# Performance work log

Hardware: AMD Instinct MI355X
Metric: run time of the kernel (lower is better)

The kernel has to match this reference:

```python
import jax, jax.numpy as jnp
import numpy as np

N_NODES = 50000
N_EDGES = 1600000
N_GRAPHS = 16
K_SLOTS = 8
LATENT = 4
HID = 32


def _linear(key, fan_in, fan_out):
    lim = 1.0 / np.sqrt(fan_in)
    kw, kb = jax.random.split(key)
    w = jax.random.uniform(kw, (fan_in, fan_out), minval=-lim, maxval=lim, dtype=jnp.float32)
    b = jax.random.uniform(kb, (fan_out,), minval=-lim, maxval=lim, dtype=jnp.float32)
    return w, b


def setup_inputs() -> dict:
    key = jax.random.key(0)
    ks = jax.random.split(key, 12)
    x = jax.random.normal(ks[0], (N_NODES, 4), dtype=jnp.float32)
    pos = jax.random.normal(ks[1], (N_NODES, 3), dtype=jnp.float32)
    # edge_index without self-loops (src != dst) so dist > 0 everywhere
    src = jax.random.randint(ks[2], (N_EDGES,), 0, N_NODES)
    off = jax.random.randint(ks[3], (N_EDGES,), 1, N_NODES)
    dst = (src + off) % N_NODES
    edge_index = jnp.stack([src, dst], axis=0).astype(jnp.int64)
    batch = jnp.sort(jax.random.randint(ks[4], (N_NODES,), 0, N_GRAPHS)).astype(jnp.int64)
    enc_w1, enc_b1 = _linear(ks[5], 4 * 2 + 1, HID)
    enc_w2, enc_b2 = _linear(ks[6], HID, HID)
    pool_w, pool_b = _linear(ks[7], HID, K_SLOTS)
    toz_w, toz_b = _linear(ks[8], HID, LATENT)
    dec_w1, dec_b1 = _linear(ks[9], LATENT, HID)
    dec_w2, dec_b2 = _linear(ks[10], HID, 4)
    return {
        "x": x, "pos": pos, "edge_index": edge_index, "batch": batch,
        "enc_w1": enc_w1, "enc_b1": enc_b1, "enc_w2": enc_w2, "enc_b2": enc_b2,
        "pool_w": pool_w, "pool_b": pool_b, "toz_w": toz_w, "toz_b": toz_b,
        "dec_w1": dec_w1, "dec_b1": dec_b1, "dec_w2": dec_w2, "dec_b2": dec_b2,
    }


def reference(x, pos, edge_index, batch,
              enc_w1, enc_b1, enc_w2, enc_b2,
              pool_w, pool_b, toz_w, toz_b,
              dec_w1, dec_b1, dec_w2, dec_b2):
    src = edge_index[0]  # x_j (source)
    dst = edge_index[1]  # x_i (target, aggregation index in PyG default flow)
    # EquiLayer: relative distance + message MLP + mean aggregation
    rel_pos = pos[src] - pos[dst]                         # [E, 3]
    dist = jnp.linalg.norm(rel_pos, axis=-1, keepdims=True)  # [E, 1]
    msg_in = jnp.concatenate([x[dst], x[src], dist], axis=-1)  # [E, 9]
    msg = jax.nn.silu(msg_in @ enc_w1 + enc_b1) @ enc_w2 + enc_b2  # [E, 32]
    summed = jax.ops.segment_sum(msg, dst, num_segments=N_NODES)   # [N, 32]
    cnt = jax.ops.segment_sum(jnp.ones((msg.shape[0], 1), msg.dtype), dst,
                              num_segments=N_NODES)
    h = summed / jnp.maximum(cnt, 1.0)                    # scatter-mean
    # soft pooling over k slots per graph
    s = jax.nn.softmax(h @ pool_w + pool_b, axis=-1)      # [N, k]
    pooled_h = jax.ops.segment_sum(s[:, :, None] * h[:, None, :], batch,
                                   num_segments=N_GRAPHS)  # [B, k, 32]
    z = pooled_h @ toz_w + toz_b                           # [B, k, latent]
    # decode: torch.matmul(s [N,k], z [B,k,d]) -> [B, N, d]
    q = jnp.einsum('nk,bkd->bnd', s, z)
    recon = jax.nn.silu(q @ dec_w1 + dec_b1) @ dec_w2 + dec_b2  # [B, N, 4]
    return recon
```

## Files before the change

### kernel.cpp

```cpp
#include <hip/hip_runtime.h>
#include <hip/hip_bf16.h>

#define N_NODES 50000
#define N_EDGES 1600000
#define N_GRAPHS 16
#define K_SLOTS 8
#define LATENT 4
#define HID 32
#define NBUCKET 196
#define BCAP 10240
#define BIN_EPB 4096

typedef __hip_bfloat16 bf16;
typedef __attribute__((ext_vector_type(8))) short short8;
typedef __attribute__((ext_vector_type(4))) float f32x4;

__device__ __forceinline__ float ldf(const void* p, long i, int isbf) {
    return isbf ? __bfloat162float(((const bf16*)p)[i]) : ((const float*)p)[i];
}
__device__ __forceinline__ int ldi(const int* p, long i, int is64) {
    return is64 ? p[2 * i] : p[i];
}
__device__ __forceinline__ short f2bs(float f) {
    bf16 h = __float2bfloat16(f);
    return *reinterpret_cast<short*>(&h);
}
__device__ __forceinline__ unsigned pk2(float a, float b) {
    __hip_bfloat162 h2 = __float22bfloat162_rn(make_float2(a, b));
    return *reinterpret_cast<unsigned*>(&h2);
}
__device__ __forceinline__ float bs2f(unsigned s) {
    union { unsigned u; float f; } cv;
    cv.u = (s & 0xFFFFu) << 16;
    return cv.f;
}
__device__ __forceinline__ float fast_silu(float v) {
    return v * __builtin_amdgcn_rcpf(1.f + __expf(-v));
}

#define WS_POOL 0
#define WS_GFILL 4096
#define WS_ZERO_CNT 4352
#define WS_HSUM 4352
#define WS_S    (WS_HSUM + N_NODES * HID)
#define WS_FRAGS (WS_S + N_NODES * K_SLOTS)
#define WS_DEG  (WS_FRAGS + 1024)
#define WS_BINNED (WS_DEG + N_NODES)
#define WS_EDAT (WS_BINNED + NBUCKET * BCAP)
#define WS_FLAGS (WS_EDAT + N_EDGES)

__global__ void prep_kernel(const void* x, const int* ei,
                            const void* w1, const void* w2,
                            int* flags, short* frags)
{
    int t = threadIdx.x;
    unsigned short h = ((const unsigned short*)x)[2 * t];
    unsigned e = (h >> 7) & 0xFF;
    bool sane = ((h & 0x7FFF) == 0 || (e >= 100 && e <= 141));
    unsigned long long bs = __ballot(sane);
    int f0 = (__popcll(bs) >= 32) ? 1 : 0;
    bool z = (ei[2 * t + 1] == 0);
    unsigned long long bz = __ballot(z);
    int f1 = (__popcll(bz) >= 60) ? 1 : 0;
    if (t == 0) { flags[0] = f0; flags[1] = f1; }

    int fbf = f0;
    int nl = t & 15, quad = (t >> 4) & 3;
#pragma unroll
    for (int j = 0; j < 8; j++) {
        int k = quad * 8 + j;
        frags[(0 * 64 + t) * 8 + j] = (k < 9) ? f2bs(ldf(w1, k * 32 + nl, fbf)) : (short)0;
        frags[(1 * 64 + t) * 8 + j] = (k < 9) ? f2bs(ldf(w1, k * 32 + 16 + nl, fbf)) : (short)0;
        frags[(2 * 64 + t) * 8 + j] = f2bs(ldf(w2, k * 32 + nl, fbf));
        frags[(3 * 64 + t) * 8 + j] = f2bs(ldf(w2, k * 32 + 16 + nl, fbf));
    }
}

__global__ __launch_bounds__(256) void bin_kernel(
    const int* __restrict__ ei, int* __restrict__ gfill,
    unsigned* __restrict__ binned, const int* __restrict__ flags)
{
    const int i64 = flags[1];
    __shared__ int cnt[NBUCKET];
    __shared__ int lbase[NBUCKET];
    __shared__ int lcur[NBUCKET];
    __shared__ int gbase[NBUCKET];
    __shared__ int tmp[256];
    __shared__ unsigned sorted[BIN_EPB];
    int t = threadIdx.x;
    for (int i = t; i < NBUCKET; i += 256) cnt[i] = 0;
    __syncthreads();

    long e0 = (long)blockIdx.x * BIN_EPB;
    unsigned pk[16];
    if (!i64) {
#pragma unroll
        for (int kk = 0; kk < 4; kk++) {
            long e = e0 + kk * 1024 + t * 4;
            if (e < N_EDGES) {
                int4 sv = *(const int4*)(ei + e);
                int4 dv = *(const int4*)(ei + N_EDGES + e);
                pk[kk * 4 + 0] = (unsigned)sv.x | ((unsigned)dv.x << 16);
                pk[kk * 4 + 1] = (unsigned)sv.y | ((unsigned)dv.y << 16);
                pk[kk * 4 + 2] = (unsigned)sv.z | ((unsigned)dv.z << 16);
                pk[kk * 4 + 3] = (unsigned)sv.w | ((unsigned)dv.w << 16);
                atomicAdd(&cnt[dv.x >> 8], 1);
                atomicAdd(&cnt[dv.y >> 8], 1);
                atomicAdd(&cnt[dv.z >> 8], 1);
                atomicAdd(&cnt[dv.w >> 8], 1);
            } else {
                pk[kk * 4 + 0] = pk[kk * 4 + 1] = pk[kk * 4 + 2] = pk[kk * 4 + 3] = 0xFFFFFFFFu;
            }
        }
    } else {
#pragma unroll
        for (int kk = 0; kk < 8; kk++) {
            long e = e0 + kk * 512 + t * 2;
            if (e < N_EDGES) {
                int4 sv = *(const int4*)(ei + 2 * e);
                int4 dv = *(const int4*)(ei + 2 * (N_EDGES + e));
                pk[kk * 2 + 0] = (unsigned)sv.x | ((unsigned)dv.x << 16);
                pk[kk * 2 + 1] = (unsigned)sv.z | ((unsigned)dv.z << 16);
                atomicAdd(&cnt[dv.x >> 8], 1);
                atomicAdd(&cnt[dv.z >> 8], 1);
            } else {
                pk[kk * 2 + 0] = pk[kk * 2 + 1] = 0xFFFFFFFFu;
            }
        }
    }
    __syncthreads();

    tmp[t] = (t < NBUCKET) ? cnt[t] : 0;
    __syncthreads();
    for (int s = 1; s < 256; s <<= 1) {
        int v = tmp[t] + ((t >= s) ? tmp[t - s] : 0);
        __syncthreads();
        tmp[t] = v;
        __syncthreads();
    }
    int total = tmp[255];
    if (t < NBUCKET) {
        int ex = tmp[t] - cnt[t];
        lbase[t] = ex;
        lcur[t] = ex;
        gbase[t] = atomicAdd(&gfill[t], cnt[t]);
    }
    __syncthreads();

#pragma unroll
    for (int k = 0; k < 16; k++) {
        if (pk[k] != 0xFFFFFFFFu) {
            int b = pk[k] >> 24;
            int p = atomicAdd(&lcur[b], 1);
            sorted[p] = pk[k];
        }
    }
    __syncthreads();

    for (int j = t; j < total; j += 256) {
        unsigned ed = sorted[j];
        int b = ed >> 24;
        binned[(long)b * BCAP + gbase[b] + (j - lbase[b])] = ed;
    }
}

__global__ __launch_bounds__(1024) void csr_kernel(
    const int* __restrict__ gfill, const unsigned* __restrict__ binned,
    unsigned* __restrict__ edat, int* __restrict__ deg, float* __restrict__ hsum)
{
    __shared__ int gsm[256];
    __shared__ int lcnt[256], lcur[256], sm[256];
    int b = blockIdx.x, t = threadIdx.x;
    if (t < 256) gsm[t] = (t < NBUCKET) ? gfill[t] : 0;
    if (t < 256) lcnt[t] = 0;
    __syncthreads();
    for (int s = 1; s < 256; s <<= 1) {
        int v = 0;
        if (t < 256) v = gsm[t] + ((t >= s) ? gsm[t - s] : 0);
        __syncthreads();
        if (t < 256) gsm[t] = v;
        __syncthreads();
    }
    {
        int nvalid = min(256, N_NODES - b * 256);
        if (nvalid > 0) {
            float4* hz = (float4*)(hsum + (size_t)b * 256 * HID);
            float4 z4 = make_float4(0.f, 0.f, 0.f, 0.f);
            for (int i = t; i < nvalid * 8; i += 1024) hz[i] = z4;
        }
    }
    int cnt = gfill[b];
    int base = gsm[b] - cnt;
    const unsigned* bp = binned + (long)b * BCAP;
    for (int i = t; i < cnt; i += 1024)
        atomicAdd(&lcnt[(bp[i] >> 16) & 255], 1);
    __syncthreads();
    if (t < 256) sm[t] = lcnt[t];
    __syncthreads();
    for (int s = 1; s < 256; s <<= 1) {
        int v = 0;
        if (t < 256) v = sm[t] + ((t >= s) ? sm[t - s] : 0);
        __syncthreads();
        if (t < 256) sm[t] = v;
        __syncthreads();
    }
    if (t < 256) {
        lcur[t] = sm[t] - lcnt[t];
        int n = b * 256 + t;
        if (n < N_NODES) deg[n] = lcnt[t];
    }
    __syncthreads();
    for (int i = t; i < cnt; i += 1024) {
        unsigned pk = bp[i];
        int pos = base + atomicAdd(&lcur[(pk >> 16) & 255], 1);
        edat[pos] = pk;
    }
}

__global__ __launch_bounds__(256) void msg_agg_kernel(
    const void* __restrict__ x, const void* __restrict__ pos,
    const unsigned* __restrict__ edat, const short* __restrict__ frags,
    const void* __restrict__ b1, const void* __restrict__ b2,
    float* __restrict__ hsum, const int* __restrict__ flags)
{
    const int fbf = flags[0];
    __shared__ short buf[256 * 34];
    __shared__ int sdL[256];
    __shared__ int runstart[256];
    __shared__ int wcnt[4];

    int t = threadIdx.x;
    int lane = t & 63, wv = t >> 6;
    int nl = lane & 15, quad = lane >> 4;

    const short8 w1f0 = *(const short8*)&frags[(0 * 64 + lane) * 8];
    const short8 w1f1 = *(const short8*)&frags[(1 * 64 + lane) * 8];
    const short8 w2f0 = *(const short8*)&frags[(2 * 64 + lane) * 8];
    const short8 w2f1 = *(const short8*)&frags[(3 * 64 + lane) * 8];
    float b1c0 = ldf(b1, nl, fbf), b1c1 = ldf(b1, 16 + nl, fbf);
    float b2c0 = ldf(b2, nl, fbf), b2c1 = ldf(b2, 16 + nl, fbf);

    long i = (long)blockIdx.x * 256 + t;
    unsigned ed = edat[i];
    int src = (int)(ed & 0xFFFFu);
    int dst = (int)(ed >> 16);
    sdL[t] = dst;

    float in[9];
    if (fbf) {
        const unsigned* xb = (const unsigned*)x;
        unsigned d0 = xb[dst * 2], d1 = xb[dst * 2 + 1];
        unsigned s0 = xb[src * 2], s1 = xb[src * 2 + 1];
        in[0] = bs2f(d0); in[1] = bs2f(d0 >> 16);
        in[2] = bs2f(d1); in[3] = bs2f(d1 >> 16);
        in[4] = bs2f(s0); in[5] = bs2f(s0 >> 16);
        in[6] = bs2f(s1); in[7] = bs2f(s1 >> 16);
        const unsigned short* pp = (const unsigned short*)pos;
        float dx = bs2f(pp[3 * src + 0]) - bs2f(pp[3 * dst + 0]);
        float dy = bs2f(pp[3 * src + 1]) - bs2f(pp[3 * dst + 1]);
        float dz = bs2f(pp[3 * src + 2]) - bs2f(pp[3 * dst + 2]);
        in[8] = sqrtf(dx * dx + dy * dy + dz * dz);
    } else {
        float4 xd = ((const float4*)x)[dst];
        float4 xs = ((const float4*)x)[src];
        in[0] = xd.x; in[1] = xd.y; in[2] = xd.z; in[3] = xd.w;
        in[4] = xs.x; in[5] = xs.y; in[6] = xs.z; in[7] = xs.w;
        const float* pf = (const float*)pos;
        float dx = pf[3 * src + 0] - pf[3 * dst + 0];
        float dy = pf[3 * src + 1] - pf[3 * dst + 1];
        float dz = pf[3 * src + 2] - pf[3 * dst + 2];
        in[8] = sqrtf(dx * dx + dy * dy + dz * dz);
    }

    {
        unsigned* rowp = (unsigned*)&buf[t * 34];
        rowp[0] = pk2(in[0], in[1]);
        rowp[1] = pk2(in[2], in[3]);
        rowp[2] = pk2(in[4], in[5]);
        rowp[3] = pk2(in[6], in[7]);
        rowp[4] = pk2(in[8], 0.f);
#pragma unroll
        for (int p = 5; p < 16; p++) rowp[p] = 0;
    }
    __syncthreads();

    int rb = wv * 64;
    short8 af[4];
#pragma unroll
    for (int mt = 0; mt < 4; mt++) {
        int row = rb + mt * 16 + nl;
        af[mt] = *(short8*)&buf[row * 34 + quad * 8];
    }
    __syncthreads();

    f32x4 zero = {0.f, 0.f, 0.f, 0.f};
#pragma unroll
    for (int mt = 0; mt < 4; mt++) {
        f32x4 c0 = __builtin_amdgcn_mfma_f32_16x16x32_bf16(af[mt], w1f0, zero, 0, 0, 0);
        f32x4 c1 = __builtin_amdgcn_mfma_f32_16x16x32_bf16(af[mt], w1f1, zero, 0, 0, 0);
#pragma unroll
        for (int r = 0; r < 4; r++) {
            int row = rb + mt * 16 + quad * 4 + r;
            buf[row * 34 + nl] = f2bs(fast_silu(c0[r] + b1c0));
            buf[row * 34 + 16 + nl] = f2bs(fast_silu(c1[r] + b1c1));
        }
    }
    __syncthreads();

    short8 a2f[4];
#pragma unroll
    for (int mt = 0; mt < 4; mt++) {
        int row = rb + mt * 16 + nl;
        a2f[mt] = *(short8*)&buf[row * 34 + quad * 8];
    }
    __syncthreads();

    short* msgT = buf;
#pragma unroll
    for (int mt = 0; mt < 4; mt++) {
        f32x4 d0 = __builtin_amdgcn_mfma_f32_16x16x32_bf16(a2f[mt], w2f0, zero, 0, 0, 0);
        f32x4 d1 = __builtin_amdgcn_mfma_f32_16x16x32_bf16(a2f[mt], w2f1, zero, 0, 0, 0);
        int ob = rb + mt * 16 + quad * 4;
        unsigned* c0p = (unsigned*)&msgT[nl * 258 + ob];
        unsigned* c1p = (unsigned*)&msgT[(nl + 16) * 258 + ob];
        c0p[0] = pk2(d0[0] + b2c0, d0[1] + b2c0);
        c0p[1] = pk2(d0[2] + b2c0, d0[3] + b2c0);
        c1p[0] = pk2(d1[0] + b2c1, d1[1] + b2c1);
        c1p[1] = pk2(d1[2] + b2c1, d1[3] + b2c1);
    }
    __syncthreads();

    bool head = (t == 0) || (sdL[t] != sdL[t - 1]);
    unsigned long long bal = __ballot(head);
    if (lane == 0) wcnt[wv] = __popcll(bal);
    __syncthreads();
    int nruns = wcnt[0] + wcnt[1] + wcnt[2] + wcnt[3];
    if (head) {
        int base = 0;
        for (int q = 0; q < wv; q++) base += wcnt[q];
        int myrun = base + __popcll(bal & (((unsigned long long)1 << lane) - 1ull));
        runstart[myrun] = t;
    }
    __syncthreads();

    int g = t >> 5, c = t & 31;
    const short* col = &msgT[c * 258];
    const unsigned* colu = (const unsigned*)col;
    for (int r = g; r < nruns; r += 8) {
        int s0 = runstart[r];
        int s1 = (r + 1 < nruns) ? runstart[r + 1] : 256;
        float acc = 0.f;
        int j = s0;
        if (j & 1) { acc += bs2f((unsigned)(unsigned short)col[j]); j++; }
        for (; j + 1 < s1; j += 2) {
            unsigned d = colu[j >> 1];
            acc += bs2f(d) + bs2f(d >> 16);
        }
        if (j < s1) acc += bs2f((unsigned)(unsigned short)col[j]);
        int node = sdL[s0];
        if (s0 == 0 || s1 == 256) atomicAdd(&hsum[(size_t)node * HID + c], acc);
        else hsum[(size_t)node * HID + c] = acc;
    }
}

__global__ __launch_bounds__(256) void pool_softmax_kernel(
    const float* __restrict__ hsum, const int* __restrict__ deg,
    const int* __restrict__ batch,
    const void* __restrict__ pw, const void* __restrict__ pb,
    float* __restrict__ s, float* __restrict__ pooled,
    const int* __restrict__ flags)
{
    const int fbf = flags[0], i64 = flags[1];
    __shared__ float spw[HID * K_SLOTS], spb[K_SLOTS];
    __shared__ float hL[256 * 33];
    __shared__ float sL[256 * 9];
    __shared__ float invL[256];
    __shared__ int gL[256];
    int t = threadIdx.x;
    int n0 = blockIdx.x * 256;
    spw[t] = ldf(pw, t, fbf);
    if (t < K_SLOTS) spb[t] = ldf(pb, t, fbf);
    {
        int n = n0 + t;
        gL[t] = ldi(batch, (n < N_NODES) ? n : (N_NODES - 1), i64);
        invL[t] = (n < N_NODES) ? __builtin_amdgcn_rcpf(fmaxf((float)deg[n], 1.f)) : 0.f;
    }
    __syncthreads();
    for (int i = t; i < 256 * HID; i += 256) {
        int row = i >> 5, col = i & 31;
        int n = n0 + row;
        hL[row * 33 + col] = (n < N_NODES) ? hsum[(size_t)n0 * HID + i] * invL[row] : 0.f;
    }
    __syncthreads();

    if (n0 + t < N_NODES) {
        float l[K_SLOTS];
#pragma unroll
        for (int k = 0; k < K_SLOTS; k++) l[k] = spb[k];
#pragma unroll
        for (int j = 0; j < HID; j++) {
            float v = hL[t * 33 + j];
#pragma unroll
            for (int k = 0; k < K_SLOTS; k++) l[k] = fmaf(v, spw[j * K_SLOTS + k], l[k]);
        }
        float mx = l[0];
#pragma unroll
        for (int k = 1; k < K_SLOTS; k++) mx = fmaxf(mx, l[k]);
        float sum = 0.f;
#pragma unroll
        for (int k = 0; k < K_SLOTS; k++) { l[k] = __expf(l[k] - mx); sum += l[k]; }
        float is = __builtin_amdgcn_rcpf(sum);
#pragma unroll
        for (int k = 0; k < K_SLOTS; k++) { l[k] *= is; sL[t * 9 + k] = l[k]; }
        float4 v0 = make_float4(l[0], l[1], l[2], l[3]);
        float4 v1 = make_float4(l[4], l[5], l[6], l[7]);
        float4* sp = (float4*)(s + (size_t)(n0 + t) * K_SLOTS);
        sp[0] = v0; sp[1] = v1;
    } else {
#pragma unroll
        for (int k = 0; k < K_SLOTS; k++) sL[t * 9 + k] = 0.f;
    }
    __syncthreads();

    int k = t >> 5, c = t & 31;
    float acc = 0.f;
    int curg = gL[0];
    int lim = min(256, N_NODES - n0);
    for (int i = 0; i < lim; i++) {
        int g = gL[i];
        if (g != curg) {
            atomicAdd(&pooled[curg * 256 + t], acc);
            acc = 0.f;
            curg = g;
        }
        acc = fmaf(sL[i * 9 + k], hL[i * 33 + c], acc);
    }
    atomicAdd(&pooled[curg * 256 + t], acc);
}

__global__ __launch_bounds__(256) void decode_kernel(
    const float* __restrict__ s, const float* __restrict__ pooled,
    const void* __restrict__ tw, const void* __restrict__ tb,
    const void* __restrict__ dw1, const void* __restrict__ db1,
    const void* __restrict__ dw2, const void* __restrict__ db2,
    void* __restrict__ out, const int* __restrict__ flags)
{
    const int fbf = flags[0];
    __shared__ float zb[K_SLOTS * LATENT];
    __shared__ float w1[LATENT * HID], b1s[HID], w2[HID * LATENT], b2s[LATENT];
    int b = blockIdx.y;
    int t = threadIdx.x;
    if (t < K_SLOTS * LATENT) {
        int k = t >> 2, d = t & 3;
        float acc = ldf(tb, d, fbf);
        for (int c = 0; c < HID; c++)
            acc = fmaf(pooled[b * 256 + k * 32 + c], ldf(tw, c * 4 + d, fbf), acc);
        zb[t] = acc;
    }
    if (t < LATENT * HID) w1[t] = ldf(dw1, t, fbf);
    else if (t < LATENT * HID + HID * LATENT) w2[t - LATENT * HID] = ldf(dw2, t - LATENT * HID, fbf);
    if (t < HID) b1s[t] = ldf(db1, t, fbf);
    if (t < LATENT) b2s[t] = ldf(db2, t, fbf);
    __syncthreads();

    int n = blockIdx.x * 256 + t;
    if (n >= N_NODES) return;
    float sv[K_SLOTS];
#pragma unroll
    for (int k = 0; k < K_SLOTS; k++) sv[k] = s[(size_t)n * K_SLOTS + k];
    float q[LATENT];
#pragma unroll
    for (int d = 0; d < LATENT; d++) {
        float a = 0.f;
#pragma unroll
        for (int k = 0; k < K_SLOTS; k++) a = fmaf(sv[k], zb[k * LATENT + d], a);
        q[d] = a;
    }
    float t1[HID];
#pragma unroll
    for (int j = 0; j < HID; j++) t1[j] = b1s[j];
#pragma unroll
    for (int d = 0; d < LATENT; d++) {
        float v = q[d];
#pragma unroll
        for (int j = 0; j < HID; j++) t1[j] = fmaf(v, w1[d * HID + j], t1[j]);
    }
#pragma unroll
    for (int j = 0; j < HID; j++) t1[j] = fast_silu(t1[j]);
    float o[LATENT];
#pragma unroll
    for (int d = 0; d < LATENT; d++) o[d] = b2s[d];
#pragma unroll
    for (int j = 0; j < HID; j++) {
        float v = t1[j];
#pragma unroll
        for (int d = 0; d < LATENT; d++) o[d] = fmaf(v, w2[j * LATENT + d], o[d]);
    }
    if (fbf) {
        union { bf16 h[4]; uint2 u; } pk;
#pragma unroll
        for (int d = 0; d < LATENT; d++) pk.h[d] = __float2bfloat16(o[d]);
        ((uint2*)out)[(size_t)b * N_NODES + n] = pk.u;
    } else {
        float4 v4 = make_float4(o[0], o[1], o[2], o[3]);
        ((float4*)out)[(size_t)b * N_NODES + n] = v4;
    }
}

extern "C" void kernel_launch(void* const* d_in, const int* in_sizes, int n_in,
                              void* d_out, int out_size, void* d_ws, size_t ws_size,
                              hipStream_t stream) {
    const void* x      = d_in[0];
    const void* pos    = d_in[1];
    const int*  ei     = (const int*)d_in[2];
    const int*  batch  = (const int*)d_in[3];
    const void* enc_w1 = d_in[4];
    const void* enc_b1 = d_in[5];
    const void* enc_w2 = d_in[6];
    const void* enc_b2 = d_in[7];
    const void* pool_w = d_in[8];
    const void* pool_b = d_in[9];
    const void* toz_w  = d_in[10];
    const void* toz_b  = d_in[11];
    const void* dec_w1 = d_in[12];
    const void* dec_b1 = d_in[13];
    const void* dec_w2 = d_in[14];
    const void* dec_b2 = d_in[15];

    float* ws = (float*)d_ws;
    float* pooled = ws + WS_POOL;
    int*   gfill  = (int*)(ws + WS_GFILL);
    float* hsum   = ws + WS_HSUM;
    float* s      = ws + WS_S;
    short* frags  = (short*)(ws + WS_FRAGS);
    int*   deg    = (int*)(ws + WS_DEG);
    unsigned* binned = (unsigned*)(ws + WS_BINNED);
    unsigned* edat   = (unsigned*)(ws + WS_EDAT);
    int*   flags  = (int*)(ws + WS_FLAGS);

    hipMemsetAsync(d_ws, 0, (size_t)WS_ZERO_CNT * 4, stream);
    prep_kernel<<<1, 64, 0, stream>>>(x, ei, enc_w1, enc_w2, flags, frags);

    int gbin = (N_EDGES + BIN_EPB - 1) / BIN_EPB;
    bin_kernel<<<gbin, 256, 0, stream>>>(ei, gfill, binned, flags);
    csr_kernel<<<NBUCKET, 1024, 0, stream>>>(gfill, binned, edat, deg, hsum);

    msg_agg_kernel<<<N_EDGES / 256, 256, 0, stream>>>(
        x, pos, edat, frags, enc_b1, enc_b2, hsum, flags);

    pool_softmax_kernel<<<NBUCKET, 256, 0, stream>>>(
        hsum, deg, batch, pool_w, pool_b, s, pooled, flags);
    dim3 dg((N_NODES + 255) / 256, N_GRAPHS);
    decode_kernel<<<dg, 256, 0, stream>>>(
        s, pooled, toz_w, toz_b, dec_w1, dec_b1, dec_w2, dec_b2, d_out, flags);
}
```

Before: 212.7 us.

## Use wave shuffle scans in binning and CSR, MFMA for pooled segment sums

The shared-memory Hillis-Steele scans in bin_kernel and csr_kernel become wavefront shuffle scans with a small cross-wave combine, which removes many block barriers. csr_kernel now gets its bucket base from a reduction over gfill entries before b, instead of a full prefix scan. pool_softmax_kernel stores h and s transposed in bf16 and computes per-graph pooled sums with 16x16x32 bf16 MFMA over segment runs found by ballot, replacing the serial per-thread loop over 256 nodes. The pooled sums now use bf16 inputs, which lowers their precision.

```diff
diff --git a/kernel.cpp b/kernel.cpp
--- a/kernel.cpp
+++ b/kernel.cpp
@@ -85,7 +85,7 @@
     __shared__ int lbase[NBUCKET];
     __shared__ int lcur[NBUCKET];
     __shared__ int gbase[NBUCKET];
-    __shared__ int tmp[256];
+    __shared__ int wsum[4];
     __shared__ unsigned sorted[BIN_EPB];
     int t = threadIdx.x;
     for (int i = t; i < NBUCKET; i += 256) cnt[i] = 0;
@@ -130,20 +130,25 @@
     }
     __syncthreads();
 
-    tmp[t] = (t < NBUCKET) ? cnt[t] : 0;
-    __syncthreads();
-    for (int s = 1; s < 256; s <<= 1) {
-        int v = tmp[t] + ((t >= s) ? tmp[t - s] : 0);
-        __syncthreads();
-        tmp[t] = v;
-        __syncthreads();
-    }
-    int total = tmp[255];
+    int cv = (t < NBUCKET) ? cnt[t] : 0;
+    int lane = t & 63;
+    int v = cv;
+#pragma unroll
+    for (int d = 1; d < 64; d <<= 1) {
+        int u = __shfl_up(v, d);
+        if (lane >= d) v += u;
+    }
+    if (lane == 63) wsum[t >> 6] = v;
+    __syncthreads();
+    int add = 0;
+    for (int q = 0; q < (t >> 6); q++) add += wsum[q];
+    int inc = v + add;
+    int total = wsum[0] + wsum[1] + wsum[2] + wsum[3];
     if (t < NBUCKET) {
-        int ex = tmp[t] - cnt[t];
+        int ex = inc - cv;
         lbase[t] = ex;
         lcur[t] = ex;
-        gbase[t] = atomicAdd(&gfill[t], cnt[t]);
+        gbase[t] = atomicAdd(&gfill[t], cv);
     }
     __syncthreads();
 
@@ -168,19 +173,19 @@
     const int* __restrict__ gfill, const unsigned* __restrict__ binned,
     unsigned* __restrict__ edat, int* __restrict__ deg, float* __restrict__ hsum)
 {
-    __shared__ int gsm[256];
-    __shared__ int lcnt[256], lcur[256], sm[256];
+    __shared__ int red[16];
+    __shared__ int lcnt[256], lcur[256];
     int b = blockIdx.x, t = threadIdx.x;
-    if (t < 256) gsm[t] = (t < NBUCKET) ? gfill[t] : 0;
+    int lane = t & 63;
     if (t < 256) lcnt[t] = 0;
-    __syncthreads();
-    for (int s = 1; s < 256; s <<= 1) {
-        int v = 0;
-        if (t < 256) v = gsm[t] + ((t >= s) ? gsm[t - s] : 0);
-        __syncthreads();
-        if (t < 256) gsm[t] = v;
-        __syncthreads();
-    }
+
+    int bv = (t < 256 && t < b && t < NBUCKET) ? gfill[t] : 0;
+#pragma unroll
+    for (int d = 32; d > 0; d >>= 1) bv += __shfl_down(bv, d);
+    if (lane == 0) red[t >> 6] = bv;
+    __syncthreads();
+    int base = red[0] + red[1] + red[2] + red[3];
+
     {
         int nvalid = min(256, N_NODES - b * 256);
         if (nvalid > 0) {
@@ -190,24 +195,27 @@
         }
     }
     int cnt = gfill[b];
-    int base = gsm[b] - cnt;
     const unsigned* bp = binned + (long)b * BCAP;
+    __syncthreads();
     for (int i = t; i < cnt; i += 1024)
         atomicAdd(&lcnt[(bp[i] >> 16) & 255], 1);
     __syncthreads();
-    if (t < 256) sm[t] = lcnt[t];
-    __syncthreads();
-    for (int s = 1; s < 256; s <<= 1) {
-        int v = 0;
-        if (t < 256) v = sm[t] + ((t >= s) ? sm[t - s] : 0);
-        __syncthreads();
-        if (t < 256) sm[t] = v;
-        __syncthreads();
-    }
+
+    int cv = (t < 256) ? lcnt[t] : 0;
+    int v = cv;
+#pragma unroll
+    for (int d = 1; d < 64; d <<= 1) {
+        int u = __shfl_up(v, d);
+        if (lane >= d) v += u;
+    }
+    if (t < 256 && lane == 63) red[t >> 6] = v;
+    __syncthreads();
     if (t < 256) {
-        lcur[t] = sm[t] - lcnt[t];
+        int add = 0;
+        for (int q = 0; q < (t >> 6); q++) add += red[q];
+        lcur[t] = v + add - cv;
         int n = b * 256 + t;
-        if (n < N_NODES) deg[n] = lcnt[t];
+        if (n < N_NODES) deg[n] = cv;
     }
     __syncthreads();
     for (int i = t; i < cnt; i += 1024) {
@@ -372,34 +380,40 @@
 {
     const int fbf = flags[0], i64 = flags[1];
     __shared__ float spw[HID * K_SLOTS], spb[K_SLOTS];
-    __shared__ float hL[256 * 33];
-    __shared__ float sL[256 * 9];
+    __shared__ short hT[32 * 266];
+    __shared__ short sT[16 * 266];
     __shared__ float invL[256];
     __shared__ int gL[256];
+    __shared__ int runstart[16];
+    __shared__ int wcnt[4];
     int t = threadIdx.x;
+    int lane = t & 63, wv = t >> 6;
     int n0 = blockIdx.x * 256;
     spw[t] = ldf(pw, t, fbf);
     if (t < K_SLOTS) spb[t] = ldf(pb, t, fbf);
+    for (int i = t; i < 8 * 266; i += 256) sT[8 * 266 + i] = 0;
     {
         int n = n0 + t;
-        gL[t] = ldi(batch, (n < N_NODES) ? n : (N_NODES - 1), i64);
-        invL[t] = (n < N_NODES) ? __builtin_amdgcn_rcpf(fmaxf((float)deg[n], 1.f)) : 0.f;
+        bool valid = n < N_NODES;
+        gL[t] = ldi(batch, valid ? n : (N_NODES - 1), i64);
+        invL[t] = valid ? __builtin_amdgcn_rcpf(fmaxf((float)deg[n], 1.f)) : 0.f;
     }
     __syncthreads();
     for (int i = t; i < 256 * HID; i += 256) {
-        int row = i >> 5, col = i & 31;
-        int n = n0 + row;
-        hL[row * 33 + col] = (n < N_NODES) ? hsum[(size_t)n0 * HID + i] * invL[row] : 0.f;
-    }
-    __syncthreads();
-
-    if (n0 + t < N_NODES) {
+        int node = i >> 5, c = i & 31;
+        float v = ((n0 + node) < N_NODES) ? hsum[(size_t)n0 * HID + i] * invL[node] : 0.f;
+        hT[c * 266 + node] = f2bs(v);
+    }
+    __syncthreads();
+
+    {
+        bool valid = (n0 + t) < N_NODES;
         float l[K_SLOTS];
 #pragma unroll
         for (int k = 0; k < K_SLOTS; k++) l[k] = spb[k];
 #pragma unroll
         for (int j = 0; j < HID; j++) {
-            float v = hL[t * 33 + j];
+            float v = bs2f((unsigned)(unsigned short)hT[j * 266 + t]);
 #pragma unroll
             for (int k = 0; k < K_SLOTS; k++) l[k] = fmaf(v, spw[j * K_SLOTS + k], l[k]);
         }
@@ -411,31 +425,65 @@
         for (int k = 0; k < K_SLOTS; k++) { l[k] = __expf(l[k] - mx); sum += l[k]; }
         float is = __builtin_amdgcn_rcpf(sum);
 #pragma unroll
-        for (int k = 0; k < K_SLOTS; k++) { l[k] *= is; sL[t * 9 + k] = l[k]; }
-        float4 v0 = make_float4(l[0], l[1], l[2], l[3]);
-        float4 v1 = make_float4(l[4], l[5], l[6], l[7]);
-        float4* sp = (float4*)(s + (size_t)(n0 + t) * K_SLOTS);
-        sp[0] = v0; sp[1] = v1;
-    } else {
-#pragma unroll
-        for (int k = 0; k < K_SLOTS; k++) sL[t * 9 + k] = 0.f;
-    }
-    __syncthreads();
-
-    int k = t >> 5, c = t & 31;
-    float acc = 0.f;
-    int curg = gL[0];
-    int lim = min(256, N_NODES - n0);
-    for (int i = 0; i < lim; i++) {
-        int g = gL[i];
-        if (g != curg) {
-            atomicAdd(&pooled[curg * 256 + t], acc);
-            acc = 0.f;
-            curg = g;
-        }
-        acc = fmaf(sL[i * 9 + k], hL[i * 33 + c], acc);
-    }
-    atomicAdd(&pooled[curg * 256 + t], acc);
+        for (int k = 0; k < K_SLOTS; k++) l[k] *= is;
+        if (valid) {
+            float4* sp = (float4*)(s + (size_t)(n0 + t) * K_SLOTS);
+            sp[0] = make_float4(l[0], l[1], l[2], l[3]);
+            sp[1] = make_float4(l[4], l[5], l[6], l[7]);
+        } else {
+#pragma unroll
+            for (int k = 0; k < K_SLOTS; k++) l[k] = 0.f;
+        }
+#pragma unroll
+        for (int k = 0; k < K_SLOTS; k++) sT[k * 266 + t] = f2bs(l[k]);
+    }
+    bool head = (t == 0) || (gL[t] != gL[t - 1]);
+    unsigned long long bal = __ballot(head);
+    if (lane == 0) wcnt[wv] = __popcll(bal);
+    __syncthreads();
+    int nruns = wcnt[0] + wcnt[1] + wcnt[2] + wcnt[3];
+    if (head) {
+        int base = 0;
+        for (int q = 0; q < wv; q++) base += wcnt[q];
+        runstart[base + __popcll(bal & (((unsigned long long)1 << lane) - 1ull))] = t;
+    }
+    __syncthreads();
+
+    int nl = lane & 15, quad = lane >> 4;
+    int wlo = wv * 64, whi = wlo + 64;
+    f32x4 zero = {0.f, 0.f, 0.f, 0.f};
+    for (int r = 0; r < nruns; r++) {
+        int lo = runstart[r];
+        int hi = (r + 1 < nruns) ? runstart[r + 1] : 256;
+        if (whi <= lo || wlo >= hi) continue;
+        bool partial = (lo > wlo) || (hi < whi);
+        f32x4 acc0 = zero, acc1 = zero;
+#pragma unroll
+        for (int kk = 0; kk < 2; kk++) {
+            int base = (wv * 2 + kk) * 32 + quad * 8;
+            short8 a = *(short8*)&sT[nl * 266 + base];
+            if (partial) {
+#pragma unroll
+                for (int j = 0; j < 8; j++) {
+                    int nd = base + j;
+                    if (nd < lo || nd >= hi) a[j] = 0;
+                }
+            }
+            short8 b0 = *(short8*)&hT[nl * 266 + base];
+            short8 b1 = *(short8*)&hT[(nl + 16) * 266 + base];
+            acc0 = __builtin_amdgcn_mfma_f32_16x16x32_bf16(a, b0, acc0, 0, 0, 0);
+            acc1 = __builtin_amdgcn_mfma_f32_16x16x32_bf16(a, b1, acc1, 0, 0, 0);
+        }
+        if (quad < 2) {
+            int g = gL[lo];
+#pragma unroll
+            for (int rr = 0; rr < 4; rr++) {
+                int k = quad * 4 + rr;
+                atomicAdd(&pooled[g * 256 + k * 32 + nl], acc0[rr]);
+                atomicAdd(&pooled[g * 256 + k * 32 + 16 + nl], acc1[rr]);
+            }
+        }
+    }
 }
 
 __global__ __launch_bounds__(256) void decode_kernel(
```

After: 200.1 us. -6.0%, faster.
